# Performance work log

Measured on AMD Instinct MI355X. Metric: run time of the kernel, lower is better.

The kernel has to match this reference:

```python
import jax, jax.numpy as jnp
import numpy as np

N, E, IN, H, OUT, L = 50000, 640000, 64, 128, 128, 4
EPS = 1e-8


def setup_inputs() -> dict:
    key = jax.random.key(0)
    ks = jax.random.split(key, 14)
    rn = lambda k, shp: (jax.random.normal(k, shp, jnp.float32) * 0.05)
    return {
        "h": jax.random.normal(ks[0], (N, IN), jnp.float32),
        "pos": jax.random.normal(ks[1], (N, 3), jnp.float32),
        "edge_index": jax.random.randint(ks[2], (2, E), 0, N),
        "emb_W": rn(ks[3], (IN, H)), "emb_b": jnp.zeros((H,), jnp.float32),
        "msg_W1": rn(ks[4], (L, 2 * H + 1, H)), "msg_b1": jnp.zeros((L, H), jnp.float32),
        "msg_W2": rn(ks[5], (L, H, H)), "msg_b2": jnp.zeros((L, H), jnp.float32),
        "coord_W1": rn(ks[6], (L, H, H)), "coord_b1": jnp.zeros((L, H), jnp.float32),
        "coord_W2": rn(ks[7], (L, H, 1)), "coord_b2": jnp.zeros((L, 1), jnp.float32),
        "node_W1": rn(ks[8], (L, 2 * H, H)), "node_b1": jnp.zeros((L, H), jnp.float32),
        "node_W2": rn(ks[9], (L, H, H)), "node_b2": jnp.zeros((L, H), jnp.float32),
        "out_W1": rn(ks[10], (H, H)), "out_b1": jnp.zeros((H,), jnp.float32),
        "out_W2": rn(ks[11], (H, OUT)), "out_b2": jnp.zeros((OUT,), jnp.float32),
    }


def _egnn_forward(h, pos, src, dst, emb_W, emb_b, msg_W1, msg_b1, msg_W2, msg_b2,
                  coord_W1, coord_b1, coord_W2, coord_b2, node_W1, node_b1,
                  node_W2, node_b2, out_W1, out_b1, out_W2, out_b2):
    n = h.shape[0]
    h = h @ emb_W + emb_b  # node embedding [N, H]
    for l in range(L):
        hi, hj = h[dst], h[src]                     # target i, source j gathers [Etot, H]
        rel = pos[src] - pos[dst]                   # row - col (used for coord update)
        dist = jnp.linalg.norm(rel, axis=-1, keepdims=True)  # symmetric, same as |pos_i - pos_j|
        # message MLP: Linear -> SiLU -> Linear -> SiLU on [h_i, h_j, dist]
        m = jax.nn.silu(jnp.concatenate([hi, hj, dist], axis=-1) @ msg_W1[l] + msg_b1[l])
        m = jax.nn.silu(m @ msg_W2[l] + msg_b2[l])
        agg = jax.ops.segment_sum(m, dst, num_segments=n)  # scatter-add to targets
        # coord update: weights from h[row]=h_j, scatter to col=dst
        w = jax.nn.silu(hj @ coord_W1[l] + coord_b1[l]) @ coord_W2[l] + coord_b2[l]  # [Etot,1]
        coord_diff = w * rel / (dist + EPS)
        pos = pos + jax.ops.segment_sum(coord_diff, dst, num_segments=n)
        # node update with residual
        nh = jax.nn.silu(jnp.concatenate([h, agg], axis=-1) @ node_W1[l] + node_b1[l]) @ node_W2[l] + node_b2[l]
        h = h + nh
    out = jax.nn.silu(h @ out_W1 + out_b1) @ out_W2 + out_b2
    return out, pos


def reference(h, pos, edge_index, emb_W, emb_b, msg_W1, msg_b1, msg_W2, msg_b2,
              coord_W1, coord_b1, coord_W2, coord_b2, node_W1, node_b1,
              node_W2, node_b2, out_W1, out_b1, out_W2, out_b2):
    n = h.shape[0]
    loops = jnp.arange(n)  # add_self_loops
    src = jnp.concatenate([edge_index[0], loops])
    dst = jnp.concatenate([edge_index[1], loops])
    return _egnn_forward(h, pos, src, dst, emb_W, emb_b, msg_W1, msg_b1, msg_W2,
                         msg_b2, coord_W1, coord_b1, coord_W2, coord_b2, node_W1,
                         node_b1, node_W2, node_b2, out_W1, out_b1, out_W2, out_b2)
```

## Files before the change

### kernel.cpp

```cpp
#include <hip/hip_runtime.h>
#include <hip/hip_bf16.h>

#define EPSV 1e-8f

typedef short bf16x8 __attribute__((ext_vector_type(8)));
typedef float f32x4  __attribute__((ext_vector_type(4)));

__device__ __forceinline__ float silu_f(float x) {
    return x / (1.0f + __expf(-x));
}
__device__ __forceinline__ float bf2f(short v) {
    return __uint_as_float(((unsigned int)(unsigned short)v) << 16);
}
__device__ __forceinline__ short f2bf(float f) {
    unsigned int u = __float_as_uint(f);
    unsigned int r = (u + 0x7fff + ((u >> 16) & 1)) >> 16;
    return (short)r;
}

#define MAXM 24
struct PackArgs {
    const float* src[MAXM];
    unsigned int doff[MAXM];
    int nchunk[MAXM];
    int nmat;
};

__global__ __launch_bounds__(256) void repack_kernel(PackArgs pa, __hip_bfloat16* base)
{
    int bid = blockIdx.x;
    int m = 0, c = bid;
    while (m < pa.nmat && c >= pa.nchunk[m]) { c -= pa.nchunk[m]; ++m; }
    const float* src = pa.src[m];
    __hip_bfloat16* dst = base + pa.doff[m] + (size_t)c * 4096;
    for (int o = threadIdx.x; o < 4096; o += 256) {
        int j = o & 7, n = (o >> 3) & 127, g = o >> 10;
        dst[o] = __float2bfloat16(src[(size_t)(c * 32 + g * 8 + j) * 128 + n]);
    }
}

__global__ __launch_bounds__(256) void hist_kernel(
    const int* __restrict__ ei, int* __restrict__ cnt, int E, int N)
{
    int e = blockIdx.x * 256 + threadIdx.x;
    int Etot = E + N;
    if (e < Etot) {
        int d = (e < E) ? ei[E + e] : (e - E);
        atomicAdd(&cnt[d], 1);
    }
}

__global__ __launch_bounds__(256) void scan_block_kernel(
    const int* __restrict__ cnt, int* __restrict__ off, int* __restrict__ part, int n)
{
    __shared__ int sdata[256];
    const int tid = threadIdx.x;
    const int base = blockIdx.x * 4096 + tid * 16;
    int loc[16]; int s = 0;
    #pragma unroll
    for (int i = 0; i < 16; ++i) {
        int idx = base + i;
        int v = (idx < n) ? cnt[idx] : 0;
        loc[i] = s; s += v;
    }
    sdata[tid] = s;
    __syncthreads();
    for (int st = 1; st < 256; st <<= 1) {
        int v = (tid >= st) ? sdata[tid - st] : 0;
        __syncthreads();
        sdata[tid] += v;
        __syncthreads();
    }
    int texc = (tid > 0) ? sdata[tid - 1] : 0;
    #pragma unroll
    for (int i = 0; i < 16; ++i) {
        int idx = base + i;
        if (idx < n) off[idx] = texc + loc[i];
    }
    if (tid == 255) part[blockIdx.x] = sdata[255];
}

__global__ void scan_part_kernel(int* part, int np)
{
    if (threadIdx.x == 0 && blockIdx.x == 0) {
        int run = 0;
        for (int i = 0; i < np; ++i) { int v = part[i]; part[i] = run; run += v; }
    }
}

__global__ __launch_bounds__(256) void scan_add_kernel(
    int* __restrict__ off, const int* __restrict__ part, int n)
{
    int idx = blockIdx.x * 4096 + threadIdx.x * 16;
    int p = part[blockIdx.x];
    #pragma unroll
    for (int i = 0; i < 16; ++i)
        if (idx + i < n) off[idx + i] += p;
}

__global__ __launch_bounds__(256) void scatter_kernel(
    const int* __restrict__ ei, int* __restrict__ off,
    int* __restrict__ esrc, int* __restrict__ edst, int E, int N)
{
    int e = blockIdx.x * 256 + threadIdx.x;
    int Etot = E + N;
    if (e < Etot) {
        int s, d;
        if (e < E) { s = ei[e]; d = ei[E + e]; }
        else       { s = d = e - E; }
        int p = atomicAdd(&off[d], 1);
        esrc[p] = s; edst[p] = d;
    }
}

template<int LDA>
__device__ __forceinline__ void mfma_gemm(const __hip_bfloat16 (*At)[LDA], int acol0,
                                          const __hip_bfloat16* __restrict__ Bp,
                                          int kchunks, int w, int lane, f32x4 acc[4][2])
{
    const int ar = lane & 15, g = lane >> 4;
    const int bc = w * 32 + (lane & 15);
    for (int c = 0; c < kchunks; ++c) {
        const int ao = acol0 + c * 32 + g * 8;
        bf16x8 a0 = *(const bf16x8*)&At[ar +  0][ao];
        bf16x8 a1 = *(const bf16x8*)&At[ar + 16][ao];
        bf16x8 a2 = *(const bf16x8*)&At[ar + 32][ao];
        bf16x8 a3 = *(const bf16x8*)&At[ar + 48][ao];
        const __hip_bfloat16* bb = Bp + ((size_t)((c * 4 + g) * 128) + bc) * 8;
        bf16x8 b0 = *(const bf16x8*)(bb);
        bf16x8 b1 = *(const bf16x8*)(bb + 128);
        acc[0][0] = __builtin_amdgcn_mfma_f32_16x16x32_bf16(a0, b0, acc[0][0], 0, 0, 0);
        acc[1][0] = __builtin_amdgcn_mfma_f32_16x16x32_bf16(a1, b0, acc[1][0], 0, 0, 0);
        acc[2][0] = __builtin_amdgcn_mfma_f32_16x16x32_bf16(a2, b0, acc[2][0], 0, 0, 0);
        acc[3][0] = __builtin_amdgcn_mfma_f32_16x16x32_bf16(a3, b0, acc[3][0], 0, 0, 0);
        acc[0][1] = __builtin_amdgcn_mfma_f32_16x16x32_bf16(a0, b1, acc[0][1], 0, 0, 0);
        acc[1][1] = __builtin_amdgcn_mfma_f32_16x16x32_bf16(a1, b1, acc[1][1], 0, 0, 0);
        acc[2][1] = __builtin_amdgcn_mfma_f32_16x16x32_bf16(a2, b1, acc[2][1], 0, 0, 0);
        acc[3][1] = __builtin_amdgcn_mfma_f32_16x16x32_bf16(a3, b1, acc[3][1], 0, 0, 0);
    }
}

__device__ __forceinline__ void zacc(f32x4 acc[4][2]) {
    #pragma unroll
    for (int r = 0; r < 4; ++r)
        #pragma unroll
        for (int c = 0; c < 2; ++c) acc[r][c] = (f32x4){0.f, 0.f, 0.f, 0.f};
}

__device__ __forceinline__ void gemm4x4(const float* __restrict__ Wg,
                                        const float* a0p, const float* a1p,
                                        const float* a2p, const float* a3p,
                                        int K, int o0, float acc[4][4]) {
    for (int k = 0; k < K; k += 4) {
        float4 a0 = *(const float4*)(a0p + k);
        float4 a1 = *(const float4*)(a1p + k);
        float4 a2 = *(const float4*)(a2p + k);
        float4 a3 = *(const float4*)(a3p + k);
        float4 w0 = *(const float4*)(Wg + (k + 0) * 128 + o0);
        float4 w1 = *(const float4*)(Wg + (k + 1) * 128 + o0);
        float4 w2 = *(const float4*)(Wg + (k + 2) * 128 + o0);
        float4 w3 = *(const float4*)(Wg + (k + 3) * 128 + o0);
        float av[4][4] = {{a0.x, a0.y, a0.z, a0.w}, {a1.x, a1.y, a1.z, a1.w},
                          {a2.x, a2.y, a2.z, a2.w}, {a3.x, a3.y, a3.z, a3.w}};
        float wv[4][4] = {{w0.x, w0.y, w0.z, w0.w}, {w1.x, w1.y, w1.z, w1.w},
                          {w2.x, w2.y, w2.z, w2.w}, {w3.x, w3.y, w3.z, w3.w}};
        #pragma unroll
        for (int i = 0; i < 4; ++i)
            #pragma unroll
            for (int kk = 0; kk < 4; ++kk)
                #pragma unroll
                for (int j = 0; j < 4; ++j)
                    acc[i][j] = fmaf(av[i][kk], wv[kk][j], acc[i][j]);
    }
}

__global__ __launch_bounds__(256) void embed_kernel(
    const float* __restrict__ hin, const float* __restrict__ W,
    const float* __restrict__ b, float* __restrict__ hbuf,
    __hip_bfloat16* __restrict__ h16, int N)
{
    __shared__ float in_tile[32][68];
    const int t = threadIdx.x;
    const int nb = blockIdx.x * 32;

    #pragma unroll
    for (int it = 0; it < 2; ++it) {
        int flat = t + 256 * it;
        int c = flat & 15, e = flat >> 4;
        int node = nb + e; if (node >= N) node = N - 1;
        *(float4*)(&in_tile[e][c * 4]) = *(const float4*)(hin + (size_t)node * 64 + c * 4);
    }
    __syncthreads();

    const int o0 = (t & 31) * 4;
    const int e0 = (t >> 5) * 4;
    float acc[4][4];
    #pragma unroll
    for (int i = 0; i < 4; ++i)
        #pragma unroll
        for (int j = 0; j < 4; ++j) acc[i][j] = 0.f;
    gemm4x4(W, &in_tile[e0][0], &in_tile[e0 + 1][0], &in_tile[e0 + 2][0], &in_tile[e0 + 3][0],
            64, o0, acc);
    float4 bv = *(const float4*)(b + o0);
    #pragma unroll
    for (int i = 0; i < 4; ++i) {
        int node = nb + e0 + i;
        if (node < N) {
            float v0 = acc[i][0] + bv.x, v1 = acc[i][1] + bv.y;
            float v2 = acc[i][2] + bv.z, v3 = acc[i][3] + bv.w;
            *(float4*)(&hbuf[(size_t)node * 128 + o0]) = make_float4(v0, v1, v2, v3);
            __hip_bfloat16* hp = h16 + (size_t)node * 128 + o0;
            hp[0] = __float2bfloat16(v0); hp[1] = __float2bfloat16(v1);
            hp[2] = __float2bfloat16(v2); hp[3] = __float2bfloat16(v3);
        }
    }
}

__global__ __launch_bounds__(256) void precompute_kernel(
    const __hip_bfloat16* __restrict__ h16,
    const __hip_bfloat16* __restrict__ W1p,
    const __hip_bfloat16* __restrict__ cW1p,
    const float* __restrict__ cb1, const float* __restrict__ cW2,
    const float* __restrict__ cb2,
    __hip_bfloat16* __restrict__ U16, __hip_bfloat16* __restrict__ V16,
    float* __restrict__ wnum, int N)
{
    __shared__ __hip_bfloat16 a8[64][136];
    __shared__ float redw[64][4];
    const int t = threadIdx.x;
    const int nb = blockIdx.x * 64;
    const int lane = t & 63, w = t >> 6, g = lane >> 4, l15 = lane & 15;

    #pragma unroll
    for (int it = 0; it < 4; ++it) {
        int flat = t + 256 * it;
        int c = flat & 15, e = flat >> 4;
        int node = nb + e; if (node >= N) node = N - 1;
        *(int4*)(&a8[e][c * 8]) = *(const int4*)(h16 + (size_t)node * 128 + c * 8);
    }
    __syncthreads();

    const int colA = w * 32 + l15, colB = colA + 16;
    f32x4 acc[4][2];

    zacc(acc);
    mfma_gemm<136>(a8, 0, W1p, 4, w, lane, acc);
    #pragma unroll
    for (int r = 0; r < 4; ++r)
        #pragma unroll
        for (int q = 0; q < 4; ++q) {
            int node = nb + r * 16 + g * 4 + q;
            if (node < N) {
                U16[(size_t)node * 128 + colA] = __float2bfloat16(acc[r][0][q]);
                U16[(size_t)node * 128 + colB] = __float2bfloat16(acc[r][1][q]);
            }
        }
    zacc(acc);
    mfma_gemm<136>(a8, 0, W1p + 4 * 4096, 4, w, lane, acc);
    #pragma unroll
    for (int r = 0; r < 4; ++r)
        #pragma unroll
        for (int q = 0; q < 4; ++q) {
            int node = nb + r * 16 + g * 4 + q;
            if (node < N) {
                V16[(size_t)node * 128 + colA] = __float2bfloat16(acc[r][0][q]);
                V16[(size_t)node * 128 + colB] = __float2bfloat16(acc[r][1][q]);
            }
        }
    zacc(acc);
    mfma_gemm<136>(a8, 0, cW1p, 4, w, lane, acc);
    {
        float cb1A = cb1[colA], cb1B = cb1[colB];
        float wA = cW2[colA], wB = cW2[colB];
        #pragma unroll
        for (int r = 0; r < 4; ++r)
            #pragma unroll
            for (int q = 0; q < 4; ++q) {
                float p = silu_f(acc[r][0][q] + cb1A) * wA
                        + silu_f(acc[r][1][q] + cb1B) * wB;
                p += __shfl_xor(p, 1);
                p += __shfl_xor(p, 2);
                p += __shfl_xor(p, 4);
                p += __shfl_xor(p, 8);
                if (l15 == 0) redw[r * 16 + g * 4 + q][w] = p;
            }
    }
    __syncthreads();
    if (t < 64 && nb + t < N)
        wnum[nb + t] = redw[t][0] + redw[t][1] + redw[t][2] + redw[t][3] + cb2[0];
}

__global__ __launch_bounds__(256) void edge_kernel(
    const __hip_bfloat16* __restrict__ U16, const __hip_bfloat16* __restrict__ V16,
    const float* __restrict__ wnum, const float* __restrict__ posb,
    const int* __restrict__ esrc, const int* __restrict__ edst,
    const float* __restrict__ W1tail, const float* __restrict__ b1,
    const __hip_bfloat16* __restrict__ W2p, const float* __restrict__ b2,
    float* __restrict__ agg, float* __restrict__ pdel, int Etot)
{
    __shared__ __hip_bfloat16 m1s[64][136];
    __shared__ int   srcl[64], dstl[64];
    __shared__ float relt[3][64], distl[64], wscl[64];

    const int t = threadIdx.x;
    const int eb = blockIdx.x * 64;
    const int lane = t & 63, w = t >> 6, g = lane >> 4, l15 = lane & 15;

    if (t < 64) {
        int e = eb + t;
        int s = 0, d = -1;
        if (e < Etot) { s = esrc[e]; d = edst[e]; }
        srcl[t] = s; dstl[t] = d;
        int dd = (d < 0) ? 0 : d;
        float rx = posb[3 * s + 0] - posb[3 * dd + 0];
        float ry = posb[3 * s + 1] - posb[3 * dd + 1];
        float rz = posb[3 * s + 2] - posb[3 * dd + 2];
        float dist = sqrtf(rx * rx + ry * ry + rz * rz);
        relt[0][t] = rx; relt[1][t] = ry; relt[2][t] = rz;
        distl[t] = dist;
        wscl[t] = wnum[s] / (dist + EPSV);
    }
    __syncthreads();

    #pragma unroll
    for (int j = 0; j < 4; ++j) {
        int f = t + 256 * j;
        int c8 = f & 15, row = f >> 4;
        bf16x8 res;
        if (dstl[row] >= 0) {
            int s = srcl[row], d = dstl[row];
            bf16x8 uv = *(const bf16x8*)(U16 + (size_t)d * 128 + c8 * 8);
            bf16x8 vv = *(const bf16x8*)(V16 + (size_t)s * 128 + c8 * 8);
            float4 wt0 = *(const float4*)(W1tail + c8 * 8);
            float4 wt1 = *(const float4*)(W1tail + c8 * 8 + 4);
            float4 bb0 = *(const float4*)(b1 + c8 * 8);
            float4 bb1 = *(const float4*)(b1 + c8 * 8 + 4);
            float dv = distl[row];
            float wt[8] = {wt0.x, wt0.y, wt0.z, wt0.w, wt1.x, wt1.y, wt1.z, wt1.w};
            float bb[8] = {bb0.x, bb0.y, bb0.z, bb0.w, bb1.x, bb1.y, bb1.z, bb1.w};
            #pragma unroll
            for (int k = 0; k < 8; ++k) {
                float x = bf2f(uv[k]) + bf2f(vv[k]) + dv * wt[k] + bb[k];
                res[k] = f2bf(silu_f(x));
            }
        } else {
            #pragma unroll
            for (int k = 0; k < 8; ++k) res[k] = 0;
        }
        *(bf16x8*)(&m1s[row][c8 * 8]) = res;
    }
    __syncthreads();

    const int colA = w * 32 + l15, colB = colA + 16;
    f32x4 acc[4][2];
    zacc(acc);
    mfma_gemm<136>(m1s, 0, W2p, 4, w, lane, acc);
    __syncthreads();

    {
        float b2a = b2[colA], b2b = b2[colB];
        #pragma unroll
        for (int r = 0; r < 4; ++r)
            #pragma unroll
            for (int q = 0; q < 4; ++q) {
                int row = r * 16 + g * 4 + q;
                m1s[row][colA] = __float2bfloat16(silu_f(acc[r][0][q] + b2a));
                m1s[row][colB] = __float2bfloat16(silu_f(acc[r][1][q] + b2b));
            }
    }
    __syncthreads();

    {
        int col = t & 127, half = t >> 7;
        int r0 = half * 32;
        float a = 0.f;
        int cur = dstl[r0];
        #pragma unroll 4
        for (int r = r0; r < r0 + 32; ++r) {
            int d = dstl[r];
            if (d != cur) {
                if (cur >= 0) atomicAdd(&agg[(size_t)cur * 128 + col], a);
                a = 0.f; cur = d;
            }
            if (d >= 0) a += bf2f(*(const short*)&m1s[r][col]);
        }
        if (cur >= 0) atomicAdd(&agg[(size_t)cur * 128 + col], a);
    }

    if (t < 192) {
        int e = t / 3, comp = t % 3;
        if (dstl[e] >= 0)
            atomicAdd(&pdel[(size_t)dstl[e] * 3 + comp], wscl[e] * relt[comp][e]);
    }
}

__global__ __launch_bounds__(256) void node_mfma_kernel(
    float* __restrict__ hbuf, __hip_bfloat16* __restrict__ h16,
    const float* __restrict__ agg,
    float* __restrict__ posb, const float* __restrict__ pdel,
    const __hip_bfloat16* __restrict__ W1p, const float* __restrict__ b1,
    const __hip_bfloat16* __restrict__ W2p, const float* __restrict__ b2,
    int N)
{
    __shared__ __hip_bfloat16 a_t[64][264];
    __shared__ __hip_bfloat16 us[64][136];
    const int t = threadIdx.x;
    const int nb = blockIdx.x * 64;
    const int lane = t & 63, w = t >> 6, g = lane >> 4;

    #pragma unroll
    for (int it = 0; it < 4; ++it) {
        int flat = t + 256 * it;
        int c = flat & 15, e = flat >> 4;
        int node = nb + e; if (node >= N) node = N - 1;
        *(int4*)(&a_t[e][c * 8]) = *(const int4*)(h16 + (size_t)node * 128 + c * 8);
    }
    #pragma unroll
    for (int it = 0; it < 8; ++it) {
        int flat = t + 256 * it;
        int c = flat & 31, e = flat >> 5;
        int node = nb + e; if (node >= N) node = N - 1;
        float4 v = *(const float4*)(agg + (size_t)node * 128 + c * 4);
        __hip_bfloat16* p = &a_t[e][128 + c * 4];
        p[0] = __float2bfloat16(v.x); p[1] = __float2bfloat16(v.y);
        p[2] = __float2bfloat16(v.z); p[3] = __float2bfloat16(v.w);
    }
    __syncthreads();

    const int colA = w * 32 + (lane & 15), colB = colA + 16;
    f32x4 acc[4][2];

    zacc(acc);
    mfma_gemm<264>(a_t, 0, W1p, 8, w, lane, acc);
    {
        float b1a = b1[colA], b1b = b1[colB];
        #pragma unroll
        for (int r = 0; r < 4; ++r)
            #pragma unroll
            for (int q = 0; q < 4; ++q) {
                int row = r * 16 + g * 4 + q;
                us[row][colA] = __float2bfloat16(silu_f(acc[r][0][q] + b1a));
                us[row][colB] = __float2bfloat16(silu_f(acc[r][1][q] + b1b));
            }
    }
    __syncthreads();

    zacc(acc);
    mfma_gemm<136>(us, 0, W2p, 4, w, lane, acc);
    {
        float b2a = b2[colA], b2b = b2[colB];
        #pragma unroll
        for (int r = 0; r < 4; ++r)
            #pragma unroll
            for (int q = 0; q < 4; ++q) {
                int row = r * 16 + g * 4 + q;
                int node = nb + row;
                if (node < N) {
                    size_t off = (size_t)node * 128;
                    float va = hbuf[off + colA] + acc[r][0][q] + b2a;
                    float vb = hbuf[off + colB] + acc[r][1][q] + b2b;
                    hbuf[off + colA] = va; hbuf[off + colB] = vb;
                    h16[off + colA] = __float2bfloat16(va);
                    h16[off + colB] = __float2bfloat16(vb);
                }
            }
    }
    if (t < 192) {
        int e = t / 3, comp = t % 3;
        int node = nb + e;
        if (node < N) posb[3 * node + comp] += pdel[3 * node + comp];
    }
}

__global__ __launch_bounds__(256) void out_mfma_kernel(
    const __hip_bfloat16* __restrict__ h16,
    const __hip_bfloat16* __restrict__ W1p, const float* __restrict__ b1,
    const __hip_bfloat16* __restrict__ W2p, const float* __restrict__ b2,
    float* __restrict__ outp, int N)
{
    __shared__ __hip_bfloat16 a8[64][136];
    __shared__ __hip_bfloat16 us[64][136];
    const int t = threadIdx.x;
    const int nb = blockIdx.x * 64;
    const int lane = t & 63, w = t >> 6, g = lane >> 4;

    #pragma unroll
    for (int it = 0; it < 4; ++it) {
        int flat = t + 256 * it;
        int c = flat & 15, e = flat >> 4;
        int node = nb + e; if (node >= N) node = N - 1;
        *(int4*)(&a8[e][c * 8]) = *(const int4*)(h16 + (size_t)node * 128 + c * 8);
    }
    __syncthreads();

    const int colA = w * 32 + (lane & 15), colB = colA + 16;
    f32x4 acc[4][2];

    zacc(acc);
    mfma_gemm<136>(a8, 0, W1p, 4, w, lane, acc);
    {
        float b1a = b1[colA], b1b = b1[colB];
        #pragma unroll
        for (int r = 0; r < 4; ++r)
            #pragma unroll
            for (int q = 0; q < 4; ++q) {
                int row = r * 16 + g * 4 + q;
                us[row][colA] = __float2bfloat16(silu_f(acc[r][0][q] + b1a));
                us[row][colB] = __float2bfloat16(silu_f(acc[r][1][q] + b1b));
            }
    }
    __syncthreads();

    zacc(acc);
    mfma_gemm<136>(us, 0, W2p, 4, w, lane, acc);
    {
        float b2a = b2[colA], b2b = b2[colB];
        #pragma unroll
        for (int r = 0; r < 4; ++r)
            #pragma unroll
            for (int q = 0; q < 4; ++q) {
                int row = r * 16 + g * 4 + q;
                int node = nb + row;
                if (node < N) {
                    outp[(size_t)node * 128 + colA] = acc[r][0][q] + b2a;
                    outp[(size_t)node * 128 + colB] = acc[r][1][q] + b2b;
                }
            }
    }
}

extern "C" void kernel_launch(void* const* d_in, const int* in_sizes, int n_in,
                              void* d_out, int out_size, void* d_ws, size_t ws_size,
                              hipStream_t stream)
{
    const float* hin  = (const float*)d_in[0];
    const float* pos  = (const float*)d_in[1];
    const int*   ei   = (const int*)d_in[2];
    const float* embW = (const float*)d_in[3];
    const float* embb = (const float*)d_in[4];
    const float* mW1  = (const float*)d_in[5];
    const float* mb1  = (const float*)d_in[6];
    const float* mW2  = (const float*)d_in[7];
    const float* mb2  = (const float*)d_in[8];
    const float* cW1  = (const float*)d_in[9];
    const float* cb1  = (const float*)d_in[10];
    const float* cW2  = (const float*)d_in[11];
    const float* cb2  = (const float*)d_in[12];
    const float* nW1  = (const float*)d_in[13];
    const float* nb1  = (const float*)d_in[14];
    const float* nW2  = (const float*)d_in[15];
    const float* nb2  = (const float*)d_in[16];
    const float* oW1  = (const float*)d_in[17];
    const float* ob1  = (const float*)d_in[18];
    const float* oW2  = (const float*)d_in[19];
    const float* ob2  = (const float*)d_in[20];

    const int N = in_sizes[0] / 64;
    const int E = in_sizes[2] / 2;
    const int Etot = E + N;

    float* hbuf = (float*)d_ws;
    float* aggb = hbuf + (size_t)N * 128;
    float* posb = aggb + (size_t)N * 128;
    float* pdel = posb + (size_t)N * 3;
    float* wnum = pdel + (size_t)N * 3;
    __hip_bfloat16* h16 = (__hip_bfloat16*)(wnum + N);
    __hip_bfloat16* U16 = h16 + (size_t)N * 128;
    __hip_bfloat16* V16 = U16 + (size_t)N * 128;
    __hip_bfloat16* packed = V16 + (size_t)N * 128;
    int* cnt  = (int*)(packed + 120 * 4096);
    int* soff = cnt + N;
    int* part = soff + N;
    int* esrc = part + 64;
    int* edst = esrc + Etot;
    float* outp = (float*)d_out;

    PackArgs pa;
    int nm = 0; unsigned int poff = 0; int totalChunks = 0;
    auto addm = [&](const float* s, int kc) {
        pa.src[nm] = s; pa.doff[nm] = poff; pa.nchunk[nm] = kc;
        poff += (unsigned int)kc * 4096; totalChunks += kc; ++nm;
    };
    for (int l = 0; l < 4; ++l) {
        addm(mW1 + (size_t)l * 257 * 128, 8);
        addm(mW2 + (size_t)l * 128 * 128, 4);
        addm(cW1 + (size_t)l * 128 * 128, 4);
        addm(nW1 + (size_t)l * 256 * 128, 8);
        addm(nW2 + (size_t)l * 128 * 128, 4);
    }
    addm(oW1, 4);
    addm(oW2, 4);
    pa.nmat = nm;

    const unsigned int LSTRIDE = 28 * 4096;

    hipMemcpyAsync(posb, pos, (size_t)N * 3 * sizeof(float),
                   hipMemcpyDeviceToDevice, stream);
    repack_kernel<<<totalChunks, 256, 0, stream>>>(pa, packed);

    const int scanBlocks = (N + 4095) / 4096;
    hipMemsetAsync(cnt, 0, (size_t)N * sizeof(int), stream);
    hist_kernel<<<(Etot + 255) / 256, 256, 0, stream>>>(ei, cnt, E, N);
    scan_block_kernel<<<scanBlocks, 256, 0, stream>>>(cnt, soff, part, N);
    scan_part_kernel<<<1, 64, 0, stream>>>(part, scanBlocks);
    scan_add_kernel<<<scanBlocks, 256, 0, stream>>>(soff, part, N);
    scatter_kernel<<<(Etot + 255) / 256, 256, 0, stream>>>(ei, soff, esrc, edst, E, N);

    const int nodeBlocks32 = (N + 31) / 32;
    const int nodeBlocks64 = (N + 63) / 64;
    const int edgeBlocks   = (Etot + 63) / 64;

    embed_kernel<<<nodeBlocks32, 256, 0, stream>>>(hin, embW, embb, hbuf, h16, N);

    precompute_kernel<<<nodeBlocks64, 256, 0, stream>>>(
        h16, packed, packed + 12 * 4096,
        cb1, cW2, cb2, U16, V16, wnum, N);

    for (int l = 0; l < 4; ++l) {
        hipMemsetAsync(aggb, 0, (size_t)N * 128 * sizeof(float), stream);
        hipMemsetAsync(pdel, 0, (size_t)N * 3 * sizeof(float), stream);
        const __hip_bfloat16* lp = packed + (size_t)l * LSTRIDE;
        edge_kernel<<<edgeBlocks, 256, 0, stream>>>(
            U16, V16, wnum, posb, esrc, edst,
            mW1 + (size_t)l * 257 * 128 + 256 * 128, mb1 + l * 128,
            lp + 8 * 4096, mb2 + l * 128,
            aggb, pdel, Etot);
        node_mfma_kernel<<<nodeBlocks64, 256, 0, stream>>>(
            hbuf, h16, aggb, posb, pdel,
            lp + 16 * 4096, nb1 + l * 128,
            lp + 24 * 4096, nb2 + l * 128, N);
        if (l < 3) {
            const __hip_bfloat16* lpn = packed + (size_t)(l + 1) * LSTRIDE;
            precompute_kernel<<<nodeBlocks64, 256, 0, stream>>>(
                h16, lpn, lpn + 12 * 4096,
                cb1 + (l + 1) * 128, cW2 + (size_t)(l + 1) * 128, cb2 + (l + 1),
                U16, V16, wnum, N);
        }
    }
    out_mfma_kernel<<<nodeBlocks64, 256, 0, stream>>>(
        h16, packed + (size_t)4 * LSTRIDE, ob1,
        packed + (size_t)4 * LSTRIDE + 4 * 4096, ob2, outp, N);

    hipMemcpyAsync(outp + (size_t)N * 128, posb, (size_t)N * 3 * sizeof(float),
                   hipMemcpyDeviceToDevice, stream);
}
```

Baseline: 1.103 ms.

## Fuse next-layer precompute into node kernel and enlarge edge tiles to 128 edges

Result: slower. 1.187 ms (+7.6%).

```diff
diff --git a/kernel.cpp b/kernel.cpp
--- a/kernel.cpp
+++ b/kernel.cpp
@@ -7,15 +7,14 @@
 typedef float f32x4  __attribute__((ext_vector_type(4)));
 
 __device__ __forceinline__ float silu_f(float x) {
-    return x / (1.0f + __expf(-x));
+    return x * __builtin_amdgcn_rcpf(1.0f + __expf(-x));
 }
 __device__ __forceinline__ float bf2f(short v) {
     return __uint_as_float(((unsigned int)(unsigned short)v) << 16);
 }
-__device__ __forceinline__ short f2bf(float f) {
-    unsigned int u = __float_as_uint(f);
-    unsigned int r = (u + 0x7fff + ((u >> 16) & 1)) >> 16;
-    return (short)r;
+__device__ __forceinline__ short f2bfs(float f) {
+    __hip_bfloat16 h = __float2bfloat16(f);
+    return *(short*)&h;
 }
 
 #define MAXM 24
@@ -219,6 +218,7 @@
 __global__ __launch_bounds__(256) void precompute_kernel(
     const __hip_bfloat16* __restrict__ h16,
     const __hip_bfloat16* __restrict__ W1p,
+    const float* __restrict__ b1,
     const __hip_bfloat16* __restrict__ cW1p,
     const float* __restrict__ cb1, const float* __restrict__ cW2,
     const float* __restrict__ cb2,
@@ -245,16 +245,19 @@
 
     zacc(acc);
     mfma_gemm<136>(a8, 0, W1p, 4, w, lane, acc);
-    #pragma unroll
-    for (int r = 0; r < 4; ++r)
-        #pragma unroll
-        for (int q = 0; q < 4; ++q) {
-            int node = nb + r * 16 + g * 4 + q;
-            if (node < N) {
-                U16[(size_t)node * 128 + colA] = __float2bfloat16(acc[r][0][q]);
-                U16[(size_t)node * 128 + colB] = __float2bfloat16(acc[r][1][q]);
-            }
-        }
+    {
+        float bA = b1[colA], bB = b1[colB];
+        #pragma unroll
+        for (int r = 0; r < 4; ++r)
+            #pragma unroll
+            for (int q = 0; q < 4; ++q) {
+                int node = nb + r * 16 + g * 4 + q;
+                if (node < N) {
+                    U16[(size_t)node * 128 + colA] = __float2bfloat16(acc[r][0][q] + bA);
+                    U16[(size_t)node * 128 + colB] = __float2bfloat16(acc[r][1][q] + bB);
+                }
+            }
+    }
     zacc(acc);
     mfma_gemm<136>(a8, 0, W1p + 4 * 4096, 4, w, lane, acc);
     #pragma unroll
@@ -290,27 +293,42 @@
         wnum[nb + t] = redw[t][0] + redw[t][1] + redw[t][2] + redw[t][3] + cb2[0];
 }
 
-__global__ __launch_bounds__(256) void edge_kernel(
+__global__ __launch_bounds__(512, 4) void edge_kernel(
     const __hip_bfloat16* __restrict__ U16, const __hip_bfloat16* __restrict__ V16,
     const float* __restrict__ wnum, const float* __restrict__ posb,
     const int* __restrict__ esrc, const int* __restrict__ edst,
-    const float* __restrict__ W1tail, const float* __restrict__ b1,
+    const float* __restrict__ W1tail,
     const __hip_bfloat16* __restrict__ W2p, const float* __restrict__ b2,
     float* __restrict__ agg, float* __restrict__ pdel, int Etot)
 {
-    __shared__ __hip_bfloat16 m1s[64][136];
-    __shared__ int   srcl[64], dstl[64];
-    __shared__ float relt[3][64], distl[64], wscl[64];
+    __shared__ __hip_bfloat16 m1s[128][136];
+    __shared__ int   dstl[128];
+    __shared__ float relt[3][128], distl[128], wscl[128];
 
     const int t = threadIdx.x;
-    const int eb = blockIdx.x * 64;
-    const int lane = t & 63, w = t >> 6, g = lane >> 4, l15 = lane & 15;
-
-    if (t < 64) {
+    const int eb = blockIdx.x * 128;
+    const int lane = t & 63, w = t >> 6;
+    const int g = lane >> 4, l15 = lane & 15;
+
+    bf16x8 uvr[4], vvr[4];
+    {
+        const int c8 = t & 15;
+        #pragma unroll
+        for (int j = 0; j < 4; ++j) {
+            int row = (t >> 4) + 32 * j;
+            int e = eb + row;
+            int s = 0, d = 0;
+            if (e < Etot) { s = esrc[e]; d = edst[e]; }
+            uvr[j] = *(const bf16x8*)(U16 + (size_t)d * 128 + c8 * 8);
+            vvr[j] = *(const bf16x8*)(V16 + (size_t)s * 128 + c8 * 8);
+        }
+    }
+
+    if (t < 128) {
         int e = eb + t;
         int s = 0, d = -1;
         if (e < Etot) { s = esrc[e]; d = edst[e]; }
-        srcl[t] = s; dstl[t] = d;
+        dstl[t] = d;
         int dd = (d < 0) ? 0 : d;
         float rx = posb[3 * s + 0] - posb[3 * dd + 0];
         float ry = posb[3 * s + 1] - posb[3 * dd + 1];
@@ -318,76 +336,75 @@
         float dist = sqrtf(rx * rx + ry * ry + rz * rz);
         relt[0][t] = rx; relt[1][t] = ry; relt[2][t] = rz;
         distl[t] = dist;
-        wscl[t] = wnum[s] / (dist + EPSV);
-    }
-    __syncthreads();
-
-    #pragma unroll
-    for (int j = 0; j < 4; ++j) {
-        int f = t + 256 * j;
-        int c8 = f & 15, row = f >> 4;
-        bf16x8 res;
-        if (dstl[row] >= 0) {
-            int s = srcl[row], d = dstl[row];
-            bf16x8 uv = *(const bf16x8*)(U16 + (size_t)d * 128 + c8 * 8);
-            bf16x8 vv = *(const bf16x8*)(V16 + (size_t)s * 128 + c8 * 8);
-            float4 wt0 = *(const float4*)(W1tail + c8 * 8);
-            float4 wt1 = *(const float4*)(W1tail + c8 * 8 + 4);
-            float4 bb0 = *(const float4*)(b1 + c8 * 8);
-            float4 bb1 = *(const float4*)(b1 + c8 * 8 + 4);
+        wscl[t] = wnum[s] * __builtin_amdgcn_rcpf(dist + EPSV);
+    }
+    __syncthreads();
+
+    {
+        const int c8 = t & 15;
+        float wt[8];
+        *(float4*)&wt[0] = *(const float4*)(W1tail + c8 * 8);
+        *(float4*)&wt[4] = *(const float4*)(W1tail + c8 * 8 + 4);
+        #pragma unroll
+        for (int j = 0; j < 4; ++j) {
+            int row = (t >> 4) + 32 * j;
             float dv = distl[row];
-            float wt[8] = {wt0.x, wt0.y, wt0.z, wt0.w, wt1.x, wt1.y, wt1.z, wt1.w};
-            float bb[8] = {bb0.x, bb0.y, bb0.z, bb0.w, bb1.x, bb1.y, bb1.z, bb1.w};
+            bf16x8 res;
             #pragma unroll
             for (int k = 0; k < 8; ++k) {
-                float x = bf2f(uv[k]) + bf2f(vv[k]) + dv * wt[k] + bb[k];
-                res[k] = f2bf(silu_f(x));
-            }
-        } else {
-            #pragma unroll
-            for (int k = 0; k < 8; ++k) res[k] = 0;
+                float x = bf2f(uvr[j][k]) + bf2f(vvr[j][k]) + dv * wt[k];
+                res[k] = f2bfs(silu_f(x));
+            }
+            *(bf16x8*)(&m1s[row][c8 * 8]) = res;
         }
-        *(bf16x8*)(&m1s[row][c8 * 8]) = res;
-    }
-    __syncthreads();
-
-    const int colA = w * 32 + l15, colB = colA + 16;
-    f32x4 acc[4][2];
-    zacc(acc);
-    mfma_gemm<136>(m1s, 0, W2p, 4, w, lane, acc);
-    __syncthreads();
-
-    {
-        float b2a = b2[colA], b2b = b2[colB];
-        #pragma unroll
-        for (int r = 0; r < 4; ++r)
-            #pragma unroll
-            for (int q = 0; q < 4; ++q) {
-                int row = r * 16 + g * 4 + q;
-                m1s[row][colA] = __float2bfloat16(silu_f(acc[r][0][q] + b2a));
-                m1s[row][colB] = __float2bfloat16(silu_f(acc[r][1][q] + b2b));
-            }
-    }
-    __syncthreads();
-
-    {
-        int col = t & 127, half = t >> 7;
-        int r0 = half * 32;
+    }
+    __syncthreads();
+
+    const int col = w * 16 + l15;
+    f32x4 acc8[8];
+    #pragma unroll
+    for (int rt = 0; rt < 8; ++rt) acc8[rt] = (f32x4){0.f, 0.f, 0.f, 0.f};
+    for (int c = 0; c < 4; ++c) {
+        const int ao = c * 32 + g * 8;
+        bf16x8 b0 = *(const bf16x8*)(W2p + ((size_t)((c * 4 + g) * 128) + col) * 8);
+        #pragma unroll
+        for (int rt = 0; rt < 8; ++rt) {
+            bf16x8 a = *(const bf16x8*)&m1s[l15 + 16 * rt][ao];
+            acc8[rt] = __builtin_amdgcn_mfma_f32_16x16x32_bf16(a, b0, acc8[rt], 0, 0, 0);
+        }
+    }
+    __syncthreads();
+
+    {
+        float b2c = b2[col];
+        #pragma unroll
+        for (int rt = 0; rt < 8; ++rt)
+            #pragma unroll
+            for (int q = 0; q < 4; ++q) {
+                int row = rt * 16 + g * 4 + q;
+                m1s[row][col] = __float2bfloat16(silu_f(acc8[rt][q] + b2c));
+            }
+    }
+    __syncthreads();
+
+    {
+        int rcol = t & 127, qtr = t >> 7;
+        int r0 = qtr * 32;
         float a = 0.f;
         int cur = dstl[r0];
         #pragma unroll 4
         for (int r = r0; r < r0 + 32; ++r) {
             int d = dstl[r];
             if (d != cur) {
-                if (cur >= 0) atomicAdd(&agg[(size_t)cur * 128 + col], a);
+                if (cur >= 0) atomicAdd(&agg[(size_t)cur * 128 + rcol], a);
                 a = 0.f; cur = d;
             }
-            if (d >= 0) a += bf2f(*(const short*)&m1s[r][col]);
+            if (d >= 0) a += bf2f(*(const short*)&m1s[r][rcol]);
         }
-        if (cur >= 0) atomicAdd(&agg[(size_t)cur * 128 + col], a);
-    }
-
-    if (t < 192) {
+        if (cur >= 0) atomicAdd(&agg[(size_t)cur * 128 + rcol], a);
+    }
+
+    if (t < 384) {
         int e = t / 3, comp = t % 3;
         if (dstl[e] >= 0)
             atomicAdd(&pdel[(size_t)dstl[e] * 3 + comp], wscl[e] * relt[comp][e]);
@@ -400,13 +417,19 @@
     float* __restrict__ posb, const float* __restrict__ pdel,
     const __hip_bfloat16* __restrict__ W1p, const float* __restrict__ b1,
     const __hip_bfloat16* __restrict__ W2p, const float* __restrict__ b2,
-    int N)
+    const __hip_bfloat16* __restrict__ nxtW1p, const float* __restrict__ nxt_b1,
+    const __hip_bfloat16* __restrict__ nxt_cW1p, const float* __restrict__ nxt_cb1,
+    const float* __restrict__ nxt_cW2, const float* __restrict__ nxt_cb2,
+    __hip_bfloat16* __restrict__ U16, __hip_bfloat16* __restrict__ V16,
+    float* __restrict__ wnum,
+    int N, int doPre)
 {
     __shared__ __hip_bfloat16 a_t[64][264];
     __shared__ __hip_bfloat16 us[64][136];
+    __shared__ float redw[64][4];
     const int t = threadIdx.x;
     const int nb = blockIdx.x * 64;
-    const int lane = t & 63, w = t >> 6, g = lane >> 4;
+    const int lane = t & 63, w = t >> 6, g = lane >> 4, l15 = lane & 15;
 
     #pragma unroll
     for (int it = 0; it < 4; ++it) {
@@ -427,7 +450,7 @@
     }
     __syncthreads();
 
-    const int colA = w * 32 + (lane & 15), colB = colA + 16;
+    const int colA = w * 32 + l15, colB = colA + 16;
     f32x4 acc[4][2];
 
     zacc(acc);
@@ -460,8 +483,12 @@
                     float va = hbuf[off + colA] + acc[r][0][q] + b2a;
                     float vb = hbuf[off + colB] + acc[r][1][q] + b2b;
                     hbuf[off + colA] = va; hbuf[off + colB] = vb;
-                    h16[off + colA] = __float2bfloat16(va);
-                    h16[off + colB] = __float2bfloat16(vb);
+                    __hip_bfloat16 ha = __float2bfloat16(va), hb = __float2bfloat16(vb);
+                    h16[off + colA] = ha; h16[off + colB] = hb;
+                    a_t[row][colA] = ha; a_t[row][colB] = hb;
+                } else {
+                    a_t[row][colA] = __float2bfloat16(0.f);
+                    a_t[row][colB] = __float2bfloat16(0.f);
                 }
             }
     }
@@ -470,6 +497,58 @@
         int node = nb + e;
         if (node < N) posb[3 * node + comp] += pdel[3 * node + comp];
     }
+
+    if (!doPre) return;
+    __syncthreads();
+
+    zacc(acc);
+    mfma_gemm<264>(a_t, 0, nxtW1p, 4, w, lane, acc);
+    {
+        float bA = nxt_b1[colA], bB = nxt_b1[colB];
+        #pragma unroll
+        for (int r = 0; r < 4; ++r)
+            #pragma unroll
+            for (int q = 0; q < 4; ++q) {
+                int node = nb + r * 16 + g * 4 + q;
+                if (node < N) {
+                    U16[(size_t)node * 128 + colA] = __float2bfloat16(acc[r][0][q] + bA);
+                    U16[(size_t)node * 128 + colB] = __float2bfloat16(acc[r][1][q] + bB);
+                }
+            }
+    }
+    zacc(acc);
+    mfma_gemm<264>(a_t, 0, nxtW1p + 4 * 4096, 4, w, lane, acc);
+    #pragma unroll
+    for (int r = 0; r < 4; ++r)
+        #pragma unroll
+        for (int q = 0; q < 4; ++q) {
+            int node = nb + r * 16 + g * 4 + q;
+            if (node < N) {
+                V16[(size_t)node * 128 + colA] = __float2bfloat16(acc[r][0][q]);
+                V16[(size_t)node * 128 + colB] = __float2bfloat16(acc[r][1][q]);
+            }
+        }
+    zacc(acc);
+    mfma_gemm<264>(a_t, 0, nxt_cW1p, 4, w, lane, acc);
+    {
+        float cb1A = nxt_cb1[colA], cb1B = nxt_cb1[colB];
+        float wA = nxt_cW2[colA], wB = nxt_cW2[colB];
+        #pragma unroll
+        for (int r = 0; r < 4; ++r)
+            #pragma unroll
+            for (int q = 0; q < 4; ++q) {
+                float p = silu_f(acc[r][0][q] + cb1A) * wA
+                        + silu_f(acc[r][1][q] + cb1B) * wB;
+                p += __shfl_xor(p, 1);
+                p += __shfl_xor(p, 2);
+                p += __shfl_xor(p, 4);
+                p += __shfl_xor(p, 8);
+                if (l15 == 0) redw[r * 16 + g * 4 + q][w] = p;
+            }
+    }
+    __syncthreads();
+    if (t < 64 && nb + t < N)
+        wnum[nb + t] = redw[t][0] + redw[t][1] + redw[t][2] + redw[t][3] + nxt_cb2[0];
 }
 
 __global__ __launch_bounds__(256) void out_mfma_kernel(
@@ -608,34 +687,34 @@
 
     const int nodeBlocks32 = (N + 31) / 32;
     const int nodeBlocks64 = (N + 63) / 64;
-    const int edgeBlocks   = (Etot + 63) / 64;
+    const int edgeBlocks   = (Etot + 127) / 128;
 
     embed_kernel<<<nodeBlocks32, 256, 0, stream>>>(hin, embW, embb, hbuf, h16, N);
 
     precompute_kernel<<<nodeBlocks64, 256, 0, stream>>>(
-        h16, packed, packed + 12 * 4096,
+        h16, packed, mb1, packed + 12 * 4096,
         cb1, cW2, cb2, U16, V16, wnum, N);
 
     for (int l = 0; l < 4; ++l) {
         hipMemsetAsync(aggb, 0, (size_t)N * 128 * sizeof(float), stream);
         hipMemsetAsync(pdel, 0, (size_t)N * 3 * sizeof(float), stream);
         const __hip_bfloat16* lp = packed + (size_t)l * LSTRIDE;
-        edge_kernel<<<edgeBlocks, 256, 0, stream>>>(
+        edge_kernel<<<edgeBlocks, 512, 0, stream>>>(
             U16, V16, wnum, posb, esrc, edst,
-            mW1 + (size_t)l * 257 * 128 + 256 * 128, mb1 + l * 128,
+            mW1 + (size_t)l * 257 * 128 + 256 * 128,
             lp + 8 * 4096, mb2 + l * 128,
             aggb, pdel, Etot);
+        const int ln = (l < 3) ? (l + 1) : l;
+        const __hip_bfloat16* lpn = packed + (size_t)ln * LSTRIDE;
         node_mfma_kernel<<<nodeBlocks64, 256, 0, stream>>>(
             hbuf, h16, aggb, posb, pdel,
             lp + 16 * 4096, nb1 + l * 128,
-            lp + 24 * 4096, nb2 + l * 128, N);
-        if (l < 3) {
-            const __hip_bfloat16* lpn = packed + (size_t)(l + 1) * LSTRIDE;
-            precompute_kernel<<<nodeBlocks64, 256, 0, stream>>>(
-                h16, lpn, lpn + 12 * 4096,
-                cb1 + (l + 1) * 128, cW2 + (size_t)(l + 1) * 128, cb2 + (l + 1),
-                U16, V16, wnum, N);
-        }
+            lp + 24 * 4096, nb2 + l * 128,
+            lpn, mb1 + (size_t)ln * 128,
+            lpn + 12 * 4096, cb1 + (size_t)ln * 128,
+            cW2 + (size_t)ln * 128, cb2 + ln,
+            U16, V16, wnum,
+            N, (l < 3) ? 1 : 0);
     }
     out_mfma_kernel<<<nodeBlocks64, 256, 0, stream>>>(
         h16, packed + (size_t)4 * LSTRIDE, ob1,
```
